# Performance work log

Measured on AMD Instinct MI355X. Metric: run time of the kernel, lower is better.

## Reference

```python
import jax, jax.numpy as jnp
import numpy as np

N = 50000      # nodes
E = 800000     # edges (before self-loops)
IN = 128       # in_channels
HID = 64       # hidden_channels
HEADS = 2
OUT = 128      # out_channels
NEG_SLOPE = 0.2


def setup_inputs() -> dict:
    key = jax.random.key(0)
    ks = jax.random.split(key, 12)
    p = lambda k, shape: jax.random.normal(k, shape, dtype=jnp.float32) * 0.05
    return {
        "x": jax.random.normal(ks[0], (N, IN), dtype=jnp.float32),
        "edge_index": jax.random.randint(ks[1], (2, E), 0, N, dtype=jnp.int32),
        "W1": p(ks[2], (IN, HEADS * HID)),
        "a_src1": p(ks[3], (HEADS, HID)),
        "a_dst1": p(ks[4], (HEADS, HID)),
        "b1": jnp.zeros((HEADS * HID,), dtype=jnp.float32),
        "W2": p(ks[5], (HEADS * HID, OUT)),
        "a_src2": p(ks[6], (1, OUT)),
        "a_dst2": p(ks[7], (1, OUT)),
        "b2": jnp.zeros((OUT,), dtype=jnp.float32),
    }


def _gat_conv(x, src, dst, W, a_src, a_dst, b, heads, out_c, concat):
    n = x.shape[0]
    h = (x @ W).reshape(n, heads, out_c)                # [N,H,C]
    al_s = jnp.sum(h * a_src, axis=-1)                  # [N,H]
    al_d = jnp.sum(h * a_dst, axis=-1)                  # [N,H]
    e = jax.nn.leaky_relu(al_s[src] + al_d[dst], NEG_SLOPE)  # [E',H]
    # softmax over edges grouped by destination node (numerically stable)
    e_max = jax.ops.segment_max(e, dst, num_segments=n)
    ee = jnp.exp(e - e_max[dst])
    denom = jax.ops.segment_sum(ee, dst, num_segments=n)
    alpha = ee / (denom[dst] + 1e-16)                   # [E',H]
    out = jax.ops.segment_sum(alpha[:, :, None] * h[src], dst, num_segments=n)  # [N,H,C]
    out = out.reshape(n, heads * out_c) if concat else out.mean(axis=1)
    return out + b


def reference(x, edge_index, W1, a_src1, a_dst1, b1, W2, a_src2, a_dst2, b2):
    n = x.shape[0]
    loops = jnp.arange(n, dtype=edge_index.dtype)       # PyG GATConv adds self-loops
    src = jnp.concatenate([edge_index[0], loops])
    dst = jnp.concatenate([edge_index[1], loops])
    h = jax.nn.elu(_gat_conv(x, src, dst, W1, a_src1, a_dst1, b1, HEADS, HID, True))
    return _gat_conv(h, src, dst, W2, a_src2, a_dst2, b2, 1, OUT, False)
```

## Files before the change

### kernel.cpp

```cpp
#include <hip/hip_runtime.h>
#include <hip/hip_bf16.h>
#include <math.h>

#define N_NODES 50000
#define NPAD 50048
#define N_EDGES 800000
#define NEG_SLOPE 0.2f
#define NBUCK ((N_NODES + 255) / 256)
#define CCHUNK 4096
#define DCAP 8192

__device__ inline float lrelu(float x) { return fmaxf(x, NEG_SLOPE * x); }

__device__ inline unsigned bf16rne(float f) {
    unsigned u = __float_as_uint(f);
    return (u + 0x7fffu + ((u >> 16) & 1u)) >> 16;
}
__device__ inline float bf2f(unsigned h) { return __uint_as_float(h << 16); }

__global__ void zerobuf_kernel(int* __restrict__ p) {
    int i = threadIdx.x;
    if (i < NBUCK) p[i] = 0;
}

__global__ __launch_bounds__(256) void bucketcount_kernel(const int* __restrict__ ei,
                                                          int* __restrict__ gbcnt) {
    __shared__ int lc[NBUCK];
    for (int i = threadIdx.x; i < NBUCK; i += 256) lc[i] = 0;
    __syncthreads();
    int stride = gridDim.x * 256;
    for (int e = blockIdx.x * 256 + threadIdx.x; e < N_EDGES; e += stride)
        atomicAdd(&lc[ei[N_EDGES + e] >> 8], 1);
    __syncthreads();
    for (int i = threadIdx.x; i < NBUCK; i += 256)
        if (lc[i]) atomicAdd(&gbcnt[i], lc[i]);
}

__global__ __launch_bounds__(256) void bucketscan_kernel(const int* __restrict__ gbcnt,
                                                         int* __restrict__ bbase,
                                                         int* __restrict__ bcur) {
    __shared__ int ss[256];
    int t = threadIdx.x;
    int v = (t < NBUCK) ? gbcnt[t] : 0;
    ss[t] = v;
    __syncthreads();
    for (int d = 1; d < 256; d <<= 1) {
        int u = (t >= d) ? ss[t - d] : 0;
        __syncthreads();
        ss[t] += u;
        __syncthreads();
    }
    int excl = ss[t] - v;
    if (t < NBUCK) { bbase[t] = excl; bcur[t] = excl; }
    if (t == 0) bbase[NBUCK] = N_EDGES;
}

__global__ __launch_bounds__(256) void bucketscatter_kernel(const int* __restrict__ ei,
                                                            int* __restrict__ bcur,
                                                            int2* __restrict__ bpairs) {
    __shared__ int cnt[NBUCK], startl[NBUCK], baseg[NBUCK], cur2[NBUCK];
    __shared__ int ss[256];
    __shared__ int2 stage[CCHUNK];
    int t = threadIdx.x;
    int e0 = blockIdx.x * CCHUNK;
    int nume = min(CCHUNK, N_EDGES - e0);
    for (int i = t; i < NBUCK; i += 256) { cnt[i] = 0; cur2[i] = 0; }
    __syncthreads();
    int src[CCHUNK / 256], dst[CCHUNK / 256];
    #pragma unroll
    for (int j = 0; j < CCHUNK / 256; ++j) {
        int idx = t + j * 256;
        if (idx < nume) {
            src[j] = ei[e0 + idx];
            dst[j] = ei[N_EDGES + e0 + idx];
            atomicAdd(&cnt[dst[j] >> 8], 1);
        } else dst[j] = -1;
    }
    __syncthreads();
    {
        int v = (t < NBUCK) ? cnt[t] : 0;
        ss[t] = v;
        __syncthreads();
        for (int d = 1; d < 256; d <<= 1) {
            int u = (t >= d) ? ss[t - d] : 0;
            __syncthreads();
            ss[t] += u;
            __syncthreads();
        }
        if (t < NBUCK) startl[t] = ss[t] - v;
    }
    __syncthreads();
    if (t < NBUCK && cnt[t] > 0) baseg[t] = atomicAdd(&bcur[t], cnt[t]);
    __syncthreads();
    #pragma unroll
    for (int j = 0; j < CCHUNK / 256; ++j) {
        if (dst[j] >= 0) {
            int b = dst[j] >> 8;
            int slot = startl[b] + atomicAdd(&cur2[b], 1);
            stage[slot] = make_int2(src[j], dst[j]);
        }
    }
    __syncthreads();
    for (int i = t; i < nume; i += 256) {
        int2 p = stage[i];
        int b = p.y >> 8;
        bpairs[baseg[b] + (i - startl[b])] = p;
    }
}

__global__ __launch_bounds__(256) void csrfinalize_kernel(const int2* __restrict__ bpairs,
                                                          const int* __restrict__ bbase,
                                                          int* __restrict__ ptr,
                                                          int* __restrict__ csr) {
    __shared__ int cnt[256], excl[256], cur[256];
    __shared__ int ss[256];
    __shared__ int2 P[DCAP];
    int b = blockIdx.x, t = threadIdx.x;
    int bb = bbase[b], be = bbase[b + 1];
    int n = be - bb;
    int d0 = b << 8;
    int dmax = min(256, N_NODES - d0);
    bool fits = (n <= DCAP);
    cnt[t] = 0; cur[t] = 0;
    __syncthreads();
    for (int i = t; i < n; i += 256) {
        int2 p = bpairs[bb + i];
        if (fits) P[i] = p;
        atomicAdd(&cnt[p.y & 255], 1);
    }
    __syncthreads();
    {
        int v = cnt[t];
        ss[t] = v;
        __syncthreads();
        for (int d = 1; d < 256; d <<= 1) {
            int u = (t >= d) ? ss[t - d] : 0;
            __syncthreads();
            ss[t] += u;
            __syncthreads();
        }
        excl[t] = ss[t] - v;
    }
    __syncthreads();
    if (t < dmax) ptr[d0 + t] = bb + excl[t];
    if (b == NBUCK - 1 && t == 0) ptr[N_NODES] = N_EDGES;
    for (int i = t; i < n; i += 256) {
        int2 p = fits ? P[i] : bpairs[bb + i];
        int ld = p.y & 255;
        int pos = bb + excl[ld] + atomicAdd(&cur[ld], 1);
        csr[pos] = p.x;
    }
}

__global__ __launch_bounds__(256) void convx_kernel(const float* __restrict__ x,
                                                    unsigned short* __restrict__ xh,
                                                    unsigned short* __restrict__ xl,
                                                    unsigned short* __restrict__ x2h,
                                                    unsigned short* __restrict__ x2l) {
    int q = blockIdx.x * 256 + threadIdx.x;
    if (q >= NPAD * 128 / 4) return;
    int e = q * 4;
    int row = e >> 7;
    float vv[4] = {0.f, 0.f, 0.f, 0.f};
    if (row < N_NODES) {
        float4 v = *(const float4*)(x + e);
        vv[0] = v.x; vv[1] = v.y; vv[2] = v.z; vv[3] = v.w;
    }
    ushort4 hh, ll;
    unsigned h0 = bf16rne(vv[0]), h1 = bf16rne(vv[1]), h2 = bf16rne(vv[2]), h3 = bf16rne(vv[3]);
    hh.x = h0; hh.y = h1; hh.z = h2; hh.w = h3;
    ll.x = bf16rne(vv[0] - bf2f(h0));
    ll.y = bf16rne(vv[1] - bf2f(h1));
    ll.z = bf16rne(vv[2] - bf2f(h2));
    ll.w = bf16rne(vv[3] - bf2f(h3));
    *(ushort4*)(xh + e) = hh;
    *(ushort4*)(xl + e) = ll;
    if (row >= N_NODES) {
        ushort4 z = {0, 0, 0, 0};
        *(ushort4*)(x2h + e) = z;
        *(ushort4*)(x2l + e) = z;
    }
}

__global__ __launch_bounds__(256) void convw_kernel(const float* __restrict__ W,
                                                    unsigned short* __restrict__ wth,
                                                    unsigned short* __restrict__ wtl) {
    int idx = blockIdx.x * 256 + threadIdx.x;
    if (idx >= 128 * 128) return;
    int c = idx >> 7, k = idx & 127;
    float v = W[(size_t)k * 128 + c];
    unsigned h = bf16rne(v);
    wth[idx] = (unsigned short)h;
    wtl[idx] = (unsigned short)bf16rne(v - bf2f(h));
}

template <int H>
__global__ __launch_bounds__(256) void gemm_mfma_kernel(const unsigned short* __restrict__ Ah,
                                                        const unsigned short* __restrict__ Al,
                                                        const unsigned short* __restrict__ Bh,
                                                        const unsigned short* __restrict__ Bl,
                                                        const float* __restrict__ asrc,
                                                        const float* __restrict__ adst,
                                                        unsigned short* __restrict__ Hb,
                                                        float* __restrict__ als,
                                                        float* __restrict__ ald,
                                                        int nrows) {
    using bf16x8 = __attribute__((ext_vector_type(8))) short;
    using f32x4  = __attribute__((ext_vector_type(4))) float;
    const int lane = threadIdx.x & 63;
    const int wv = threadIdx.x >> 6;
    const int l15 = lane & 15;
    const int g = lane >> 4;
    const int lk = g * 8;
    const int rowbase = blockIdx.x * 128 + wv * 32;

    f32x4 acc[2][8];
    #pragma unroll
    for (int rt = 0; rt < 2; ++rt)
        #pragma unroll
        for (int ct = 0; ct < 8; ++ct) acc[rt][ct] = (f32x4){0.f, 0.f, 0.f, 0.f};

    #pragma unroll
    for (int kc = 0; kc < 4; ++kc) {
        const int ko = kc * 32 + lk;
        bf16x8 ah0 = *(const bf16x8*)(Ah + (size_t)(rowbase + l15) * 128 + ko);
        bf16x8 ah1 = *(const bf16x8*)(Ah + (size_t)(rowbase + 16 + l15) * 128 + ko);
        bf16x8 al0 = *(const bf16x8*)(Al + (size_t)(rowbase + l15) * 128 + ko);
        bf16x8 al1 = *(const bf16x8*)(Al + (size_t)(rowbase + 16 + l15) * 128 + ko);
        #pragma unroll
        for (int ct = 0; ct < 8; ++ct) {
            bf16x8 bh = *(const bf16x8*)(Bh + (size_t)(ct * 16 + l15) * 128 + ko);
            bf16x8 bl = *(const bf16x8*)(Bl + (size_t)(ct * 16 + l15) * 128 + ko);
            acc[0][ct] = __builtin_amdgcn_mfma_f32_16x16x32_bf16(ah0, bh, acc[0][ct], 0, 0, 0);
            acc[0][ct] = __builtin_amdgcn_mfma_f32_16x16x32_bf16(ah0, bl, acc[0][ct], 0, 0, 0);
            acc[0][ct] = __builtin_amdgcn_mfma_f32_16x16x32_bf16(al0, bh, acc[0][ct], 0, 0, 0);
            acc[1][ct] = __builtin_amdgcn_mfma_f32_16x16x32_bf16(ah1, bh, acc[1][ct], 0, 0, 0);
            acc[1][ct] = __builtin_amdgcn_mfma_f32_16x16x32_bf16(ah1, bl, acc[1][ct], 0, 0, 0);
            acc[1][ct] = __builtin_amdgcn_mfma_f32_16x16x32_bf16(al1, bh, acc[1][ct], 0, 0, 0);
        }
    }

    float as8[8], ad8[8];
    #pragma unroll
    for (int ct = 0; ct < 8; ++ct) { as8[ct] = asrc[ct * 16 + l15]; ad8[ct] = adst[ct * 16 + l15]; }

    #pragma unroll
    for (int rt = 0; rt < 2; ++rt) {
        #pragma unroll
        for (int ct = 0; ct < 8; ++ct) {
            #pragma unroll
            for (int j = 0; j < 4; ++j) {
                int row = rowbase + rt * 16 + g * 4 + j;
                if (row < nrows)
                    Hb[(size_t)row * 128 + ct * 16 + l15] = (unsigned short)bf16rne(acc[rt][ct][j]);
            }
        }
        #pragma unroll
        for (int j = 0; j < 4; ++j) {
            int row = rowbase + rt * 16 + g * 4 + j;
            if (H == 2) {
                float sp0 = 0.f, sp1 = 0.f, dp0 = 0.f, dp1 = 0.f;
                #pragma unroll
                for (int ct = 0; ct < 4; ++ct) { sp0 += acc[rt][ct][j] * as8[ct]; dp0 += acc[rt][ct][j] * ad8[ct]; }
                #pragma unroll
                for (int ct = 4; ct < 8; ++ct) { sp1 += acc[rt][ct][j] * as8[ct]; dp1 += acc[rt][ct][j] * ad8[ct]; }
                #pragma unroll
                for (int off = 1; off < 16; off <<= 1) {
                    sp0 += __shfl_xor(sp0, off); sp1 += __shfl_xor(sp1, off);
                    dp0 += __shfl_xor(dp0, off); dp1 += __shfl_xor(dp1, off);
                }
                if (l15 == 0 && row < nrows) {
                    als[(size_t)row * 2]     = sp0; als[(size_t)row * 2 + 1] = sp1;
                    ald[(size_t)row * 2]     = dp0; ald[(size_t)row * 2 + 1] = dp1;
                }
            } else {
                float sp = 0.f, dp = 0.f;
                #pragma unroll
                for (int ct = 0; ct < 8; ++ct) { sp += acc[rt][ct][j] * as8[ct]; dp += acc[rt][ct][j] * ad8[ct]; }
                #pragma unroll
                for (int off = 1; off < 16; off <<= 1) {
                    sp += __shfl_xor(sp, off); dp += __shfl_xor(dp, off);
                }
                if (l15 == 0 && row < nrows) { als[row] = sp; ald[row] = dp; }
            }
        }
    }
}

template <int H, int DO_ELU, int BSPLIT>
__global__ __launch_bounds__(256) void aggregate_kernel(const unsigned short* __restrict__ Hb,
                                                        const float* __restrict__ als,
                                                        const float* __restrict__ aldv,
                                                        const int* __restrict__ ptr,
                                                        const int* __restrict__ csr,
                                                        const float* __restrict__ bias,
                                                        float* __restrict__ out,
                                                        unsigned short* __restrict__ oh,
                                                        unsigned short* __restrict__ ol) {
    __shared__ int   s_src[4][64];
    __shared__ float s_p[4][H][64];
    const int w = threadIdx.x >> 6;
    const int lane = threadIdx.x & 63;
    const int d = blockIdx.x * 4 + w;
    if (d >= N_NODES) return;
    const int head = (H == 2) ? (lane >> 5) : 0;

    int beg = ptr[d], end = ptr[d + 1];

    float ald0, ald1 = 0.f, es0, es1 = 0.f;
    if (H == 2) {
        float2 ta = *(const float2*)(aldv + (size_t)d * 2);
        float2 ts = *(const float2*)(als + (size_t)d * 2);
        ald0 = ta.x; ald1 = ta.y;
        es0 = lrelu(ts.x + ald0); es1 = lrelu(ts.y + ald1);
    } else {
        ald0 = aldv[d]; es0 = lrelu(als[d] + ald0);
    }

    int k0 = beg + lane;
    int src0 = 0;
    float e0 = -INFINITY, e1 = -INFINITY;
    if (k0 < end) {
        src0 = csr[k0];
        if (H == 2) {
            float2 t = *(const float2*)(als + (size_t)src0 * 2);
            e0 = lrelu(t.x + ald0); e1 = lrelu(t.y + ald1);
        } else e0 = lrelu(als[src0] + ald0);
    }
    float m0 = fmaxf(es0, e0);
    float m1 = (H == 2) ? fmaxf(es1, e1) : 0.f;
    for (int k = k0 + 64; k < end; k += 64) {
        int s = csr[k];
        if (H == 2) {
            float2 t = *(const float2*)(als + (size_t)s * 2);
            m0 = fmaxf(m0, lrelu(t.x + ald0));
            m1 = fmaxf(m1, lrelu(t.y + ald1));
        } else m0 = fmaxf(m0, lrelu(als[s] + ald0));
    }
    #pragma unroll
    for (int off = 32; off; off >>= 1) {
        m0 = fmaxf(m0, __shfl_xor(m0, off));
        if (H == 2) m1 = fmaxf(m1, __shfl_xor(m1, off));
    }

    float l0 = 0.f, l1 = 0.f;
    float ax0 = 0.f, ay0 = 0.f, ax1 = 0.f, ay1 = 0.f;
    float ax2 = 0.f, ay2 = 0.f, ax3 = 0.f, ay3 = 0.f;

    for (int t0 = beg; t0 < end; t0 += 64) {
        int cnt = min(64, end - t0);
        int k = t0 + lane;
        if (k < end) {
            int s; float f0, f1 = 0.f;
            if (t0 == beg) { s = src0; f0 = e0; f1 = e1; }
            else {
                s = csr[k];
                if (H == 2) {
                    float2 t = *(const float2*)(als + (size_t)s * 2);
                    f0 = lrelu(t.x + ald0); f1 = lrelu(t.y + ald1);
                } else f0 = lrelu(als[s] + ald0);
            }
            float p0 = __expf(f0 - m0);
            l0 += p0;
            s_src[w][lane] = s;
            s_p[w][0][lane] = p0;
            if (H == 2) {
                float p1 = __expf(f1 - m1);
                l1 += p1;
                s_p[w][1][lane] = p1;
            }
        }
        int j = 0;
        for (; j + 3 < cnt; j += 4) {
            int sA = s_src[w][j],     sB = s_src[w][j + 1];
            int sC = s_src[w][j + 2], sD = s_src[w][j + 3];
            float pA = s_p[w][head][j],     pB = s_p[w][head][j + 1];
            float pC = s_p[w][head][j + 2], pD = s_p[w][head][j + 3];
            unsigned uA = ((const unsigned*)(Hb + (size_t)sA * 128))[lane];
            unsigned uB = ((const unsigned*)(Hb + (size_t)sB * 128))[lane];
            unsigned uC = ((const unsigned*)(Hb + (size_t)sC * 128))[lane];
            unsigned uD = ((const unsigned*)(Hb + (size_t)sD * 128))[lane];
            ax0 = fmaf(pA, __uint_as_float(uA << 16), ax0);
            ay0 = fmaf(pA, __uint_as_float(uA & 0xffff0000u), ay0);
            ax1 = fmaf(pB, __uint_as_float(uB << 16), ax1);
            ay1 = fmaf(pB, __uint_as_float(uB & 0xffff0000u), ay1);
            ax2 = fmaf(pC, __uint_as_float(uC << 16), ax2);
            ay2 = fmaf(pC, __uint_as_float(uC & 0xffff0000u), ay2);
            ax3 = fmaf(pD, __uint_as_float(uD << 16), ax3);
            ay3 = fmaf(pD, __uint_as_float(uD & 0xffff0000u), ay3);
        }
        for (; j < cnt; ++j) {
            int sA = s_src[w][j];
            float pA = s_p[w][head][j];
            unsigned uA = ((const unsigned*)(Hb + (size_t)sA * 128))[lane];
            ax0 = fmaf(pA, __uint_as_float(uA << 16), ax0);
            ay0 = fmaf(pA, __uint_as_float(uA & 0xffff0000u), ay0);
        }
    }

    float ax = (ax0 + ax1) + (ax2 + ax3);
    float ay = (ay0 + ay1) + (ay2 + ay3);
    float mh  = (head == 0) ? m0 : m1;
    float esh = (head == 0) ? es0 : es1;
    float psh = __expf(esh - mh);
    {
        unsigned u = ((const unsigned*)(Hb + (size_t)d * 128))[lane];
        ax = fmaf(psh, __uint_as_float(u << 16), ax);
        ay = fmaf(psh, __uint_as_float(u & 0xffff0000u), ay);
    }
    #pragma unroll
    for (int off = 32; off; off >>= 1) {
        l0 += __shfl_xor(l0, off);
        if (H == 2) l1 += __shfl_xor(l1, off);
    }
    float denom = ((head == 0) ? l0 : l1) + psh;
    float inv = 1.f / (denom + 1e-16f);
    float o0 = ax * inv + bias[2 * lane];
    float o1 = ay * inv + bias[2 * lane + 1];
    if (DO_ELU) {
        o0 = o0 > 0.f ? o0 : expm1f(o0);
        o1 = o1 > 0.f ? o1 : expm1f(o1);
    }
    if (BSPLIT) {
        unsigned h0 = bf16rne(o0), h1 = bf16rne(o1);
        ushort2 sh; sh.x = h0; sh.y = h1;
        ushort2 sl; sl.x = bf16rne(o0 - bf2f(h0)); sl.y = bf16rne(o1 - bf2f(h1));
        *(ushort2*)(oh + (size_t)d * 128 + 2 * lane) = sh;
        *(ushort2*)(ol + (size_t)d * 128 + 2 * lane) = sl;
    } else {
        ((float2*)(out + (size_t)d * 128))[lane] = make_float2(o0, o1);
    }
}

extern "C" void kernel_launch(void* const* d_in, const int* in_sizes, int n_in,
                              void* d_out, int out_size, void* d_ws, size_t ws_size,
                              hipStream_t stream) {
    const float* x      = (const float*)d_in[0];
    const int*   ei     = (const int*)d_in[1];
    const float* W1     = (const float*)d_in[2];
    const float* a_src1 = (const float*)d_in[3];
    const float* a_dst1 = (const float*)d_in[4];
    const float* b1     = (const float*)d_in[5];
    const float* W2     = (const float*)d_in[6];
    const float* a_src2 = (const float*)d_in[7];
    const float* a_dst2 = (const float*)d_in[8];
    const float* b2     = (const float*)d_in[9];
    float* out = (float*)d_out;

    char* ws = (char*)d_ws;
    size_t off = 0;
    auto alloc = [&](size_t bytes) { void* p = ws + off; off += (bytes + 255) & ~(size_t)255; return p; };
    int*   ptr    = (int*)alloc((N_NODES + 1) * sizeof(int));
    int*   gbcnt  = (int*)alloc(NBUCK * sizeof(int));
    int*   bbase  = (int*)alloc((NBUCK + 1) * sizeof(int));
    int*   bcur   = (int*)alloc(NBUCK * sizeof(int));
    int2*  bpairs = (int2*)alloc((size_t)N_EDGES * sizeof(int2));
    int*   csr    = (int*)alloc(N_EDGES * sizeof(int));
    unsigned short* xbh = (unsigned short*)alloc((size_t)NPAD * 128 * 2);
    unsigned short* xbl = (unsigned short*)alloc((size_t)NPAD * 128 * 2);
    unsigned short* x2h = (unsigned short*)alloc((size_t)NPAD * 128 * 2);
    unsigned short* x2l = (unsigned short*)alloc((size_t)NPAD * 128 * 2);
    unsigned short* hb  = (unsigned short*)alloc((size_t)N_NODES * 128 * 2);
    unsigned short* w1h = (unsigned short*)alloc(128 * 128 * 2);
    unsigned short* w1l = (unsigned short*)alloc(128 * 128 * 2);
    unsigned short* w2h = (unsigned short*)alloc(128 * 128 * 2);
    unsigned short* w2l = (unsigned short*)alloc(128 * 128 * 2);
    float* als    = (float*)alloc(N_NODES * 2 * sizeof(float));
    float* ald    = (float*)alloc(N_NODES * 2 * sizeof(float));

    zerobuf_kernel<<<1, 256, 0, stream>>>(gbcnt);
    bucketcount_kernel<<<256, 256, 0, stream>>>(ei, gbcnt);
    bucketscan_kernel<<<1, 256, 0, stream>>>(gbcnt, bbase, bcur);
    bucketscatter_kernel<<<(N_EDGES + CCHUNK - 1) / CCHUNK, 256, 0, stream>>>(ei, bcur, bpairs);
    csrfinalize_kernel<<<NBUCK, 256, 0, stream>>>(bpairs, bbase, ptr, csr);

    convx_kernel<<<(NPAD * 128 / 4 + 255) / 256, 256, 0, stream>>>(x, xbh, xbl, x2h, x2l);
    convw_kernel<<<64, 256, 0, stream>>>(W1, w1h, w1l);
    convw_kernel<<<64, 256, 0, stream>>>(W2, w2h, w2l);

    int gblocks = NPAD / 128;
    int wblocks = (N_NODES + 3) / 4;

    gemm_mfma_kernel<2><<<gblocks, 256, 0, stream>>>(xbh, xbl, w1h, w1l, a_src1, a_dst1, hb, als, ald, N_NODES);
    aggregate_kernel<2, 1, 1><<<wblocks, 256, 0, stream>>>(hb, als, ald, ptr, csr, b1, nullptr, x2h, x2l);

    gemm_mfma_kernel<1><<<gblocks, 256, 0, stream>>>(x2h, x2l, w2h, w2l, a_src2, a_dst2, hb, als, ald, N_NODES);
    aggregate_kernel<1, 0, 0><<<wblocks, 256, 0, stream>>>(hb, als, ald, ptr, csr, b2, out, nullptr, nullptr);
}
```

Measured before the change: 185.3 us.

## Gather four neighbor rows per wave with 16-byte loads in aggregation

The aggregation loop is restructured so each 16-lane quarter of a wave handles a different neighbor edge, and each lane loads 8 bf16 features with a uint4 load instead of 2 with a 32-bit load. Partial sums are combined across quarters with cross-lane shuffles, and only the first quarter writes the output row with vector stores. The goal is fewer, wider gather instructions and more edges in flight per iteration. The cost is 8 accumulators per lane, a reduction shuffle, and wasted lanes when the neighbor count is not a multiple of 4.

```diff
diff --git a/kernel.cpp b/kernel.cpp
--- a/kernel.cpp
+++ b/kernel.cpp
@@ -303,7 +303,10 @@
     const int lane = threadIdx.x & 63;
     const int d = blockIdx.x * 4 + w;
     if (d >= N_NODES) return;
-    const int head = (H == 2) ? (lane >> 5) : 0;
+    const int l15 = lane & 15;
+    const int quarter = lane >> 4;
+    const int headA = (H == 2) ? (lane >> 5) : 0;
+    const int headB = (H == 2) ? (l15 >> 3) : 0;
 
     int beg = ptr[d], end = ptr[d + 1];
 
@@ -344,8 +347,9 @@
     }
 
     float l0 = 0.f, l1 = 0.f;
-    float ax0 = 0.f, ay0 = 0.f, ax1 = 0.f, ay1 = 0.f;
-    float ax2 = 0.f, ay2 = 0.f, ax3 = 0.f, ay3 = 0.f;
+    float acc[8];
+    #pragma unroll
+    for (int i = 0; i < 8; ++i) acc[i] = 0.f;
 
     for (int t0 = beg; t0 < end; t0 += 64) {
         int cnt = min(64, end - t0);
@@ -370,65 +374,79 @@
                 s_p[w][1][lane] = p1;
             }
         }
-        int j = 0;
-        for (; j + 3 < cnt; j += 4) {
-            int sA = s_src[w][j],     sB = s_src[w][j + 1];
-            int sC = s_src[w][j + 2], sD = s_src[w][j + 3];
-            float pA = s_p[w][head][j],     pB = s_p[w][head][j + 1];
-            float pC = s_p[w][head][j + 2], pD = s_p[w][head][j + 3];
-            unsigned uA = ((const unsigned*)(Hb + (size_t)sA * 128))[lane];
-            unsigned uB = ((const unsigned*)(Hb + (size_t)sB * 128))[lane];
-            unsigned uC = ((const unsigned*)(Hb + (size_t)sC * 128))[lane];
-            unsigned uD = ((const unsigned*)(Hb + (size_t)sD * 128))[lane];
-            ax0 = fmaf(pA, __uint_as_float(uA << 16), ax0);
-            ay0 = fmaf(pA, __uint_as_float(uA & 0xffff0000u), ay0);
-            ax1 = fmaf(pB, __uint_as_float(uB << 16), ax1);
-            ay1 = fmaf(pB, __uint_as_float(uB & 0xffff0000u), ay1);
-            ax2 = fmaf(pC, __uint_as_float(uC << 16), ax2);
-            ay2 = fmaf(pC, __uint_as_float(uC & 0xffff0000u), ay2);
-            ax3 = fmaf(pD, __uint_as_float(uD << 16), ax3);
-            ay3 = fmaf(pD, __uint_as_float(uD & 0xffff0000u), ay3);
-        }
-        for (; j < cnt; ++j) {
-            int sA = s_src[w][j];
-            float pA = s_p[w][head][j];
-            unsigned uA = ((const unsigned*)(Hb + (size_t)sA * 128))[lane];
-            ax0 = fmaf(pA, __uint_as_float(uA << 16), ax0);
-            ay0 = fmaf(pA, __uint_as_float(uA & 0xffff0000u), ay0);
-        }
-    }
-
-    float ax = (ax0 + ax1) + (ax2 + ax3);
-    float ay = (ay0 + ay1) + (ay2 + ay3);
-    float mh  = (head == 0) ? m0 : m1;
-    float esh = (head == 0) ? es0 : es1;
+        for (int j = 0; j < cnt; j += 4) {
+            int eidx = min(j + quarter, cnt - 1);
+            float pq = (j + quarter < cnt) ? s_p[w][headB][eidx] : 0.f;
+            int sq = s_src[w][eidx];
+            uint4 u = *(const uint4*)(Hb + (size_t)sq * 128 + 8 * l15);
+            acc[0] = fmaf(pq, __uint_as_float(u.x << 16), acc[0]);
+            acc[1] = fmaf(pq, __uint_as_float(u.x & 0xffff0000u), acc[1]);
+            acc[2] = fmaf(pq, __uint_as_float(u.y << 16), acc[2]);
+            acc[3] = fmaf(pq, __uint_as_float(u.y & 0xffff0000u), acc[3]);
+            acc[4] = fmaf(pq, __uint_as_float(u.z << 16), acc[4]);
+            acc[5] = fmaf(pq, __uint_as_float(u.z & 0xffff0000u), acc[5]);
+            acc[6] = fmaf(pq, __uint_as_float(u.w << 16), acc[6]);
+            acc[7] = fmaf(pq, __uint_as_float(u.w & 0xffff0000u), acc[7]);
+        }
+    }
+
+    #pragma unroll
+    for (int i = 0; i < 8; ++i) {
+        acc[i] += __shfl_xor(acc[i], 16);
+        acc[i] += __shfl_xor(acc[i], 32);
+    }
+    float mh  = (headB == 0) ? m0 : m1;
+    float esh = (headB == 0) ? es0 : es1;
     float psh = __expf(esh - mh);
     {
-        unsigned u = ((const unsigned*)(Hb + (size_t)d * 128))[lane];
-        ax = fmaf(psh, __uint_as_float(u << 16), ax);
-        ay = fmaf(psh, __uint_as_float(u & 0xffff0000u), ay);
+        uint4 u = *(const uint4*)(Hb + (size_t)d * 128 + 8 * l15);
+        acc[0] = fmaf(psh, __uint_as_float(u.x << 16), acc[0]);
+        acc[1] = fmaf(psh, __uint_as_float(u.x & 0xffff0000u), acc[1]);
+        acc[2] = fmaf(psh, __uint_as_float(u.y << 16), acc[2]);
+        acc[3] = fmaf(psh, __uint_as_float(u.y & 0xffff0000u), acc[3]);
+        acc[4] = fmaf(psh, __uint_as_float(u.z << 16), acc[4]);
+        acc[5] = fmaf(psh, __uint_as_float(u.z & 0xffff0000u), acc[5]);
+        acc[6] = fmaf(psh, __uint_as_float(u.w << 16), acc[6]);
+        acc[7] = fmaf(psh, __uint_as_float(u.w & 0xffff0000u), acc[7]);
     }
     #pragma unroll
     for (int off = 32; off; off >>= 1) {
         l0 += __shfl_xor(l0, off);
         if (H == 2) l1 += __shfl_xor(l1, off);
     }
-    float denom = ((head == 0) ? l0 : l1) + psh;
+    float denom = ((headB == 0) ? l0 : l1) + psh;
     float inv = 1.f / (denom + 1e-16f);
-    float o0 = ax * inv + bias[2 * lane];
-    float o1 = ay * inv + bias[2 * lane + 1];
+    float o[8];
+    float4 b4a = *(const float4*)(bias + 8 * l15);
+    float4 b4b = *(const float4*)(bias + 8 * l15 + 4);
+    o[0] = acc[0] * inv + b4a.x; o[1] = acc[1] * inv + b4a.y;
+    o[2] = acc[2] * inv + b4a.z; o[3] = acc[3] * inv + b4a.w;
+    o[4] = acc[4] * inv + b4b.x; o[5] = acc[5] * inv + b4b.y;
+    o[6] = acc[6] * inv + b4b.z; o[7] = acc[7] * inv + b4b.w;
     if (DO_ELU) {
-        o0 = o0 > 0.f ? o0 : expm1f(o0);
-        o1 = o1 > 0.f ? o1 : expm1f(o1);
-    }
-    if (BSPLIT) {
-        unsigned h0 = bf16rne(o0), h1 = bf16rne(o1);
-        ushort2 sh; sh.x = h0; sh.y = h1;
-        ushort2 sl; sl.x = bf16rne(o0 - bf2f(h0)); sl.y = bf16rne(o1 - bf2f(h1));
-        *(ushort2*)(oh + (size_t)d * 128 + 2 * lane) = sh;
-        *(ushort2*)(ol + (size_t)d * 128 + 2 * lane) = sl;
-    } else {
-        ((float2*)(out + (size_t)d * 128))[lane] = make_float2(o0, o1);
+        #pragma unroll
+        for (int i = 0; i < 8; ++i) o[i] = o[i] > 0.f ? o[i] : expm1f(o[i]);
+    }
+    if (quarter == 0) {
+        if (BSPLIT) {
+            ushort4 sh0, sh1, sl0, sl1;
+            unsigned h;
+            h = bf16rne(o[0]); sh0.x = h; sl0.x = bf16rne(o[0] - bf2f(h));
+            h = bf16rne(o[1]); sh0.y = h; sl0.y = bf16rne(o[1] - bf2f(h));
+            h = bf16rne(o[2]); sh0.z = h; sl0.z = bf16rne(o[2] - bf2f(h));
+            h = bf16rne(o[3]); sh0.w = h; sl0.w = bf16rne(o[3] - bf2f(h));
+            h = bf16rne(o[4]); sh1.x = h; sl1.x = bf16rne(o[4] - bf2f(h));
+            h = bf16rne(o[5]); sh1.y = h; sl1.y = bf16rne(o[5] - bf2f(h));
+            h = bf16rne(o[6]); sh1.z = h; sl1.z = bf16rne(o[6] - bf2f(h));
+            h = bf16rne(o[7]); sh1.w = h; sl1.w = bf16rne(o[7] - bf2f(h));
+            *(ushort4*)(oh + (size_t)d * 128 + 8 * l15)     = sh0;
+            *(ushort4*)(oh + (size_t)d * 128 + 8 * l15 + 4) = sh1;
+            *(ushort4*)(ol + (size_t)d * 128 + 8 * l15)     = sl0;
+            *(ushort4*)(ol + (size_t)d * 128 + 8 * l15 + 4) = sl1;
+        } else {
+            *(float4*)(out + (size_t)d * 128 + 8 * l15)     = make_float4(o[0], o[1], o[2], o[3]);
+            *(float4*)(out + (size_t)d * 128 + 8 * l15 + 4) = make_float4(o[4], o[5], o[6], o[7]);
+        }
     }
 }
 
```

After: 193.1 us. 1.04x slower.

## Pack edge indices to 16-bit and fuse fp32 split-conversion into first GEMM

Applied to the files above, without the earlier changes.

Edge (src,dst) pairs are packed into one 32-bit word during bucketing, and the CSR column array is stored as 16-bit indices. This relies on N being below 65536 and cuts the bytes moved in the CSR build and in edge gathering. The separate x conversion kernel is removed: the first GEMM now reads fp32 x directly and splits it into bf16 hi/lo pairs in registers, which saves a full write and re-read of the converted input. ELU now uses __expf-1 instead of expm1f, and the padding rows of x2h/x2l are no longer zeroed, which could leave garbage in padded GEMM rows that are later discarded.

```diff
diff --git a/kernel.cpp b/kernel.cpp
--- a/kernel.cpp
+++ b/kernel.cpp
@@ -57,10 +57,10 @@
 
 __global__ __launch_bounds__(256) void bucketscatter_kernel(const int* __restrict__ ei,
                                                             int* __restrict__ bcur,
-                                                            int2* __restrict__ bpairs) {
+                                                            unsigned* __restrict__ bpairs) {
     __shared__ int cnt[NBUCK], startl[NBUCK], baseg[NBUCK], cur2[NBUCK];
     __shared__ int ss[256];
-    __shared__ int2 stage[CCHUNK];
+    __shared__ unsigned stage[CCHUNK];
     int t = threadIdx.x;
     int e0 = blockIdx.x * CCHUNK;
     int nume = min(CCHUNK, N_EDGES - e0);
@@ -97,24 +97,24 @@
         if (dst[j] >= 0) {
             int b = dst[j] >> 8;
             int slot = startl[b] + atomicAdd(&cur2[b], 1);
-            stage[slot] = make_int2(src[j], dst[j]);
+            stage[slot] = (unsigned)src[j] | ((unsigned)dst[j] << 16);
         }
     }
     __syncthreads();
     for (int i = t; i < nume; i += 256) {
-        int2 p = stage[i];
-        int b = p.y >> 8;
-        bpairs[baseg[b] + (i - startl[b])] = p;
-    }
-}
-
-__global__ __launch_bounds__(256) void csrfinalize_kernel(const int2* __restrict__ bpairs,
+        unsigned pk = stage[i];
+        int b = pk >> 24;
+        bpairs[baseg[b] + (i - startl[b])] = pk;
+    }
+}
+
+__global__ __launch_bounds__(256) void csrfinalize_kernel(const unsigned* __restrict__ bpairs,
                                                           const int* __restrict__ bbase,
                                                           int* __restrict__ ptr,
-                                                          int* __restrict__ csr) {
+                                                          unsigned short* __restrict__ csr) {
     __shared__ int cnt[256], excl[256], cur[256];
     __shared__ int ss[256];
-    __shared__ int2 P[DCAP];
+    __shared__ unsigned P[DCAP];
     int b = blockIdx.x, t = threadIdx.x;
     int bb = bbase[b], be = bbase[b + 1];
     int n = be - bb;
@@ -124,9 +124,9 @@
     cnt[t] = 0; cur[t] = 0;
     __syncthreads();
     for (int i = t; i < n; i += 256) {
-        int2 p = bpairs[bb + i];
-        if (fits) P[i] = p;
-        atomicAdd(&cnt[p.y & 255], 1);
+        unsigned pk = bpairs[bb + i];
+        if (fits) P[i] = pk;
+        atomicAdd(&cnt[(pk >> 16) & 255], 1);
     }
     __syncthreads();
     {
@@ -145,40 +145,10 @@
     if (t < dmax) ptr[d0 + t] = bb + excl[t];
     if (b == NBUCK - 1 && t == 0) ptr[N_NODES] = N_EDGES;
     for (int i = t; i < n; i += 256) {
-        int2 p = fits ? P[i] : bpairs[bb + i];
-        int ld = p.y & 255;
+        unsigned pk = fits ? P[i] : bpairs[bb + i];
+        int ld = (pk >> 16) & 255;
         int pos = bb + excl[ld] + atomicAdd(&cur[ld], 1);
-        csr[pos] = p.x;
-    }
-}
-
-__global__ __launch_bounds__(256) void convx_kernel(const float* __restrict__ x,
-                                                    unsigned short* __restrict__ xh,
-                                                    unsigned short* __restrict__ xl,
-                                                    unsigned short* __restrict__ x2h,
-                                                    unsigned short* __restrict__ x2l) {
-    int q = blockIdx.x * 256 + threadIdx.x;
-    if (q >= NPAD * 128 / 4) return;
-    int e = q * 4;
-    int row = e >> 7;
-    float vv[4] = {0.f, 0.f, 0.f, 0.f};
-    if (row < N_NODES) {
-        float4 v = *(const float4*)(x + e);
-        vv[0] = v.x; vv[1] = v.y; vv[2] = v.z; vv[3] = v.w;
-    }
-    ushort4 hh, ll;
-    unsigned h0 = bf16rne(vv[0]), h1 = bf16rne(vv[1]), h2 = bf16rne(vv[2]), h3 = bf16rne(vv[3]);
-    hh.x = h0; hh.y = h1; hh.z = h2; hh.w = h3;
-    ll.x = bf16rne(vv[0] - bf2f(h0));
-    ll.y = bf16rne(vv[1] - bf2f(h1));
-    ll.z = bf16rne(vv[2] - bf2f(h2));
-    ll.w = bf16rne(vv[3] - bf2f(h3));
-    *(ushort4*)(xh + e) = hh;
-    *(ushort4*)(xl + e) = ll;
-    if (row >= N_NODES) {
-        ushort4 z = {0, 0, 0, 0};
-        *(ushort4*)(x2h + e) = z;
-        *(ushort4*)(x2l + e) = z;
+        csr[pos] = (unsigned short)(pk & 0xFFFFu);
     }
 }
 
@@ -194,9 +164,10 @@
     wtl[idx] = (unsigned short)bf16rne(v - bf2f(h));
 }
 
-template <int H>
+template <int H, int AF32>
 __global__ __launch_bounds__(256) void gemm_mfma_kernel(const unsigned short* __restrict__ Ah,
                                                         const unsigned short* __restrict__ Al,
+                                                        const float* __restrict__ Af,
                                                         const unsigned short* __restrict__ Bh,
                                                         const unsigned short* __restrict__ Bl,
                                                         const float* __restrict__ asrc,
@@ -213,6 +184,8 @@
     const int g = lane >> 4;
     const int lk = g * 8;
     const int rowbase = blockIdx.x * 128 + wv * 32;
+    const int r0c = min(rowbase + l15, nrows - 1);
+    const int r1c = min(rowbase + 16 + l15, nrows - 1);
 
     f32x4 acc[2][8];
     #pragma unroll
@@ -223,10 +196,27 @@
     #pragma unroll
     for (int kc = 0; kc < 4; ++kc) {
         const int ko = kc * 32 + lk;
-        bf16x8 ah0 = *(const bf16x8*)(Ah + (size_t)(rowbase + l15) * 128 + ko);
-        bf16x8 ah1 = *(const bf16x8*)(Ah + (size_t)(rowbase + 16 + l15) * 128 + ko);
-        bf16x8 al0 = *(const bf16x8*)(Al + (size_t)(rowbase + l15) * 128 + ko);
-        bf16x8 al1 = *(const bf16x8*)(Al + (size_t)(rowbase + 16 + l15) * 128 + ko);
+        bf16x8 ah0, ah1, al0, al1;
+        if constexpr (AF32) {
+            const float* b0 = Af + (size_t)r0c * 128 + ko;
+            const float* b1 = Af + (size_t)r1c * 128 + ko;
+            float4 u0 = *(const float4*)b0, u1 = *(const float4*)(b0 + 4);
+            float4 v0 = *(const float4*)b1, v1 = *(const float4*)(b1 + 4);
+            float a0[8] = {u0.x, u0.y, u0.z, u0.w, u1.x, u1.y, u1.z, u1.w};
+            float a1[8] = {v0.x, v0.y, v0.z, v0.w, v1.x, v1.y, v1.z, v1.w};
+            #pragma unroll
+            for (int i = 0; i < 8; ++i) {
+                unsigned h0 = bf16rne(a0[i]);
+                ah0[i] = (short)h0; al0[i] = (short)bf16rne(a0[i] - bf2f(h0));
+                unsigned h1 = bf16rne(a1[i]);
+                ah1[i] = (short)h1; al1[i] = (short)bf16rne(a1[i] - bf2f(h1));
+            }
+        } else {
+            ah0 = *(const bf16x8*)(Ah + (size_t)(rowbase + l15) * 128 + ko);
+            ah1 = *(const bf16x8*)(Ah + (size_t)(rowbase + 16 + l15) * 128 + ko);
+            al0 = *(const bf16x8*)(Al + (size_t)(rowbase + l15) * 128 + ko);
+            al1 = *(const bf16x8*)(Al + (size_t)(rowbase + 16 + l15) * 128 + ko);
+        }
         #pragma unroll
         for (int ct = 0; ct < 8; ++ct) {
             bf16x8 bh = *(const bf16x8*)(Bh + (size_t)(ct * 16 + l15) * 128 + ko);
@@ -292,7 +282,7 @@
                                                         const float* __restrict__ als,
                                                         const float* __restrict__ aldv,
                                                         const int* __restrict__ ptr,
-                                                        const int* __restrict__ csr,
+                                                        const unsigned short* __restrict__ csr,
                                                         const float* __restrict__ bias,
                                                         float* __restrict__ out,
                                                         unsigned short* __restrict__ oh,
@@ -418,8 +408,8 @@
     float o0 = ax * inv + bias[2 * lane];
     float o1 = ay * inv + bias[2 * lane + 1];
     if (DO_ELU) {
-        o0 = o0 > 0.f ? o0 : expm1f(o0);
-        o1 = o1 > 0.f ? o1 : expm1f(o1);
+        o0 = o0 > 0.f ? o0 : __expf(o0) - 1.f;
+        o1 = o1 > 0.f ? o1 : __expf(o1) - 1.f;
     }
     if (BSPLIT) {
         unsigned h0 = bf16rne(o0), h1 = bf16rne(o1);
@@ -450,14 +440,12 @@
     char* ws = (char*)d_ws;
     size_t off = 0;
     auto alloc = [&](size_t bytes) { void* p = ws + off; off += (bytes + 255) & ~(size_t)255; return p; };
-    int*   ptr    = (int*)alloc((N_NODES + 1) * sizeof(int));
-    int*   gbcnt  = (int*)alloc(NBUCK * sizeof(int));
-    int*   bbase  = (int*)alloc((NBUCK + 1) * sizeof(int));
-    int*   bcur   = (int*)alloc(NBUCK * sizeof(int));
-    int2*  bpairs = (int2*)alloc((size_t)N_EDGES * sizeof(int2));
-    int*   csr    = (int*)alloc(N_EDGES * sizeof(int));
-    unsigned short* xbh = (unsigned short*)alloc((size_t)NPAD * 128 * 2);
-    unsigned short* xbl = (unsigned short*)alloc((size_t)NPAD * 128 * 2);
+    int*      ptr    = (int*)alloc((N_NODES + 1) * sizeof(int));
+    int*      gbcnt  = (int*)alloc(NBUCK * sizeof(int));
+    int*      bbase  = (int*)alloc((NBUCK + 1) * sizeof(int));
+    int*      bcur   = (int*)alloc(NBUCK * sizeof(int));
+    unsigned* bpairs = (unsigned*)alloc((size_t)N_EDGES * sizeof(unsigned));
+    unsigned short* csr = (unsigned short*)alloc((size_t)N_EDGES * sizeof(unsigned short));
     unsigned short* x2h = (unsigned short*)alloc((size_t)NPAD * 128 * 2);
     unsigned short* x2l = (unsigned short*)alloc((size_t)NPAD * 128 * 2);
     unsigned short* hb  = (unsigned short*)alloc((size_t)N_NODES * 128 * 2);
@@ -474,16 +462,19 @@
     bucketscatter_kernel<<<(N_EDGES + CCHUNK - 1) / CCHUNK, 256, 0, stream>>>(ei, bcur, bpairs);
     csrfinalize_kernel<<<NBUCK, 256, 0, stream>>>(bpairs, bbase, ptr, csr);
 
-    convx_kernel<<<(NPAD * 128 / 4 + 255) / 256, 256, 0, stream>>>(x, xbh, xbl, x2h, x2l);
     convw_kernel<<<64, 256, 0, stream>>>(W1, w1h, w1l);
     convw_kernel<<<64, 256, 0, stream>>>(W2, w2h, w2l);
 
     int gblocks = NPAD / 128;
     int wblocks = (N_NODES + 3) / 4;
 
-    gemm_mfma_kernel<2><<<gblocks, 256, 0, stream>>>(xbh, xbl, w1h, w1l, a_src1, a_dst1, hb, als, ald, N_NODES);
-    aggregate_kernel<2, 1, 1><<<wblocks, 256, 0, stream>>>(hb, als, ald, ptr, csr, b1, nullptr, x2h, x2l);
-
-    gemm_mfma_kernel<1><<<gblocks, 256, 0, stream>>>(x2h, x2l, w2h, w2l, a_src2, a_dst2, hb, als, ald, N_NODES);
-    aggregate_kernel<1, 0, 0><<<wblocks, 256, 0, stream>>>(hb, als, ald, ptr, csr, b2, out, nullptr, nullptr);
-}
+    gemm_mfma_kernel<2, 1><<<gblocks, 256, 0, stream>>>(nullptr, nullptr, x, w1h, w1l,
+                                                        a_src1, a_dst1, hb, als, ald, N_NODES);
+    aggregate_kernel<2, 1, 1><<<wblocks, 256, 0, stream>>>(hb, als, ald, ptr, csr, b1,
+                                                           nullptr, x2h, x2l);
+
+    gemm_mfma_kernel<1, 0><<<gblocks, 256, 0, stream>>>(x2h, x2l, nullptr, w2h, w2l,
+                                                        a_src2, a_dst2, hb, als, ald, N_NODES);
+    aggregate_kernel<1, 0, 0><<<wblocks, 256, 0, stream>>>(hb, als, ald, ptr, csr, b2,
+                                                           out, nullptr, nullptr);
+}
```

Result: faster. 174.6 us (-5.8%).
